# Optimization experiments

Hardware: AMD Instinct MI355X
Metric: run time of the kernel (lower is better)

The kernel has to match this reference:

```python
import jax, jax.numpy as jnp
import numpy as np

NUM_NODES = 100000
NUM_RELS = 500
DIM = 64          # input_dim == hidden_dim == output_dim
NUM_EDGES = 1_000_000
LEAKY_SLOPE = 0.01  # torch F.leaky_relu default


def _linear_params(key, fin, fout):
    # torch nn.Linear default init: U(-1/sqrt(fin), 1/sqrt(fin))
    kw, kb = jax.random.split(key)
    s = 1.0 / np.sqrt(fin)
    W = jax.random.uniform(kw, (fout, fin), minval=-s, maxval=s, dtype=jnp.float32)
    b = jax.random.uniform(kb, (fout,), minval=-s, maxval=s, dtype=jnp.float32)
    return W, b


def setup_inputs() -> dict:
    key = jax.random.key(0)
    ks = jax.random.split(key, 12)
    src_idx = jax.random.randint(ks[0], (NUM_EDGES,), 0, NUM_NODES, dtype=jnp.int32)
    dst_idx = jax.random.randint(ks[1], (NUM_EDGES,), 0, NUM_NODES, dtype=jnp.int32)
    rel_idx = jax.random.randint(ks[2], (NUM_EDGES,), 0, NUM_RELS, dtype=jnp.int32)
    ent_embed = jax.random.normal(ks[3], (NUM_NODES, DIM), dtype=jnp.float32)
    rel_embed = jax.random.normal(ks[4], (NUM_RELS, DIM), dtype=jnp.float32)
    W_ent, b_ent = _linear_params(ks[5], DIM, DIM)          # fc_ent
    W_relL, b_relL = _linear_params(ks[6], DIM, DIM)        # fc_rel
    W_rel2, b_rel2 = _linear_params(ks[7], DIM, DIM)        # fc_rel2
    W_rel3, b_rel3 = _linear_params(ks[8], 3 * DIM, DIM)    # fc_rel3
    W_a, b_a = _linear_params(ks[9], DIM, 1)                # a
    W_fc, b_fc = _linear_params(ks[10], 3 * DIM, DIM)       # fc
    return {
        "ent_embed": ent_embed, "rel_embed": rel_embed,
        "W_ent": W_ent, "b_ent": b_ent,
        "W_relL": W_relL, "b_relL": b_relL,
        "W_rel2": W_rel2, "b_rel2": b_rel2,
        "W_rel3": W_rel3, "b_rel3": b_rel3,
        "W_a": W_a, "b_a": b_a,
        "W_fc": W_fc, "b_fc": b_fc,
        "src_idx": src_idx, "dst_idx": dst_idx, "rel_idx": rel_idx,
    }


def reference(ent_embed, rel_embed, W_ent, b_ent, W_relL, b_relL,
              W_rel2, b_rel2, W_rel3, b_rel3, W_a, b_a, W_fc, b_fc,
              src_idx, dst_idx, rel_idx):
    # --- per-edge projections (first=True path: lookup from learned tables) ---
    src = ent_embed[src_idx] @ W_ent.T + b_ent            # [E, D]
    dst = ent_embed[dst_idx] @ W_ent.T + b_ent            # [E, D]
    rel = rel_embed[rel_idx] @ W_relL.T + b_relL          # [E, D]

    # --- edge message c and unnormalized attention b ---
    c = jnp.concatenate([src, dst, rel], axis=1) @ W_fc.T + b_fc   # [E, D]
    logits = jax.nn.leaky_relu((c @ W_a.T + b_a)[:, 0], LEAKY_SLOPE)  # [E]
    b = jnp.exp(logits)                                    # [E] (original uses plain exp)

    # --- scatter-softmax over edges grouped by source node ---
    b_sum = jax.ops.segment_sum(b, src_idx, num_segments=NUM_NODES)  # [N]
    alpha = b / b_sum[src_idx]                             # [E]

    # --- attention-weighted neighbor aggregation ---
    h_ent = jax.ops.segment_sum(alpha[:, None] * c, src_idx,
                                num_segments=NUM_NODES)    # [N, D]

    # --- relation pooling: mean over edges of each relation ---
    rel2 = rel @ W_rel2.T + b_rel2                         # [E, D]
    feats = jnp.concatenate([h_ent[src_idx], h_ent[dst_idx], rel2], axis=1)  # [E, 3D]
    sums = jax.ops.segment_sum(feats, rel_idx, num_segments=NUM_RELS)        # [R, 3D]
    counts = jax.ops.segment_sum(jnp.ones_like(b), rel_idx, num_segments=NUM_RELS)
    mean = sums / jnp.maximum(counts, 1.0)[:, None]        # [R, 3D]

    h_rel = mean @ W_rel3.T + b_rel3                       # [R, D]
    return (h_ent, h_rel)
```

## Files before the change

kernel.cpp:

```cpp
#include <hip/hip_runtime.h>
#include <hip/hip_fp16.h>
#include <math.h>

#define N_NODES 100000
#define N_RELS  500
#define DIM     64
#define N_EDGES 1000000
#define SLOPE   0.01f
#define RSUB    16
#define SC_EDGES 2048
#define NB_E    489
#define NBKT    196
#define BSH     9
#define NROWS   (N_RELS + NBKT)
#define BMAX    5632

__device__ __forceinline__ unsigned short f2bf(float f) {
    unsigned int u = __float_as_uint(f);
    u += 0x7FFFu + ((u >> 16) & 1u);
    return (unsigned short)(u >> 16);
}
__device__ __forceinline__ float bfl(unsigned int u) { return __uint_as_float(u << 16); }
__device__ __forceinline__ float bfh(unsigned int u) { return __uint_as_float(u & 0xFFFF0000u); }

__device__ __forceinline__ unsigned int f2e5m2(float f) {
    __half h = __float2half_rn(f);
    unsigned short hu;
    __builtin_memcpy(&hu, &h, 2);
    unsigned int u = hu;
    u += 0x7Fu + ((u >> 8) & 1u);
    return (u >> 8) & 0xFFu;
}
__device__ __forceinline__ float e5d(unsigned int b) {
    unsigned short u = (unsigned short)(b << 8);
    __half h;
    __builtin_memcpy(&h, &u, 2);
    return __half2float(h);
}
__device__ __forceinline__ void acc8(float* a, uint2 w) {
    unsigned int x = w.x, y = w.y;
    a[0] += e5d(x & 255u);         a[1] += e5d((x >> 8) & 255u);
    a[2] += e5d((x >> 16) & 255u); a[3] += e5d(x >> 24);
    a[4] += e5d(y & 255u);         a[5] += e5d((y >> 8) & 255u);
    a[6] += e5d((y >> 16) & 255u); a[7] += e5d(y >> 24);
}

__global__ void k_fold(const float* __restrict__ W_ent, const float* __restrict__ b_ent,
                       const float* __restrict__ W_relL, const float* __restrict__ b_relL,
                       const float* __restrict__ W_rel2, const float* __restrict__ b_rel2,
                       const float* __restrict__ W_fc, const float* __restrict__ b_fc,
                       float* __restrict__ Wcat, float* __restrict__ dcat,
                       float* __restrict__ MW, float* __restrict__ MQ,
                       float* __restrict__ dW, float* __restrict__ dQ) {
    int idx = blockIdx.x * 256 + threadIdx.x;
    if (idx < 8192) {
        int k = idx >> 7;
        int j2 = idx & 127;
        int jj = j2 & 63;
        int off = (j2 >> 6) * 64;
        float s = 0.f;
        for (int i = 0; i < 64; i++) s += W_fc[jj*192 + off + i] * W_ent[i*64 + k];
        Wcat[k*128 + j2] = s;
    } else if (idx < 12288) {
        int rem = idx - 8192;
        int j = rem >> 6, i = rem & 63;
        float s = 0.f;
        for (int k = 0; k < 64; k++) s += W_fc[j*192 + 128 + k] * W_relL[k*64 + i];
        MW[j*64 + i] = s;
    } else if (idx < 16384) {
        int rem = idx - 12288;
        int j = rem >> 6, i = rem & 63;
        float s = 0.f;
        for (int k = 0; k < 64; k++) s += W_rel2[j*64 + k] * W_relL[k*64 + i];
        MQ[j*64 + i] = s;
    } else if (idx < 16512) {
        int j2 = idx - 16384;
        int jj = j2 & 63;
        int off = (j2 >> 6) * 64;
        float s = 0.f;
        for (int i = 0; i < 64; i++) s += b_ent[i] * W_fc[jj*192 + off + i];
        dcat[j2] = s;
    } else if (idx < 16640) {
        int rem = idx - 16512;
        int vec = rem >> 6, j = rem & 63;
        if (vec == 0) {
            float s = b_fc[j];
            for (int k = 0; k < 64; k++) s += b_relL[k] * W_fc[j*192 + 128 + k];
            dW[j] = s;
        } else {
            float s = b_rel2[j];
            for (int k = 0; k < 64; k++) s += b_relL[k] * W_rel2[j*64 + k];
            dQ[j] = s;
        }
    }
}

__global__ __launch_bounds__(256) void k_node(const float* __restrict__ ent,
        const float* __restrict__ Wcat, const float* __restrict__ dcat,
        const float* __restrict__ W_a,
        float* __restrict__ Uout, unsigned short* __restrict__ V16,
        float* __restrict__ us, float* __restrict__ vs) {
    __shared__ float sA[64][68];
    __shared__ float sW[64][128];
    int t = threadIdx.x;
    int tile0 = blockIdx.x * 64;
    for (int i = t; i < 2048; i += 256)
        ((float4*)sW)[i] = ((const float4*)Wcat)[i];
    for (int f = t; f < 1024; f += 256) {
        int n = f >> 4, k4 = f & 15;
        float4 v4 = (tile0 + n < N_NODES)
            ? ((const float4*)(ent + (size_t)(tile0 + n) * 64))[k4]
            : make_float4(0.f, 0.f, 0.f, 0.f);
        *(float4*)&sA[n][k4 * 4] = v4;
    }
    __syncthreads();

    int ng = t >> 4;
    int jg = t & 15;
    int n0 = ng * 4;
    int j0 = jg * 8;

    float4 d0 = *(const float4*)(dcat + j0);
    float4 d1 = *(const float4*)(dcat + j0 + 4);
    float acc[4][8];
    #pragma unroll
    for (int a = 0; a < 4; a++) {
        acc[a][0] = d0.x; acc[a][1] = d0.y; acc[a][2] = d0.z; acc[a][3] = d0.w;
        acc[a][4] = d1.x; acc[a][5] = d1.y; acc[a][6] = d1.z; acc[a][7] = d1.w;
    }

    #pragma unroll 4
    for (int k = 0; k < 64; k++) {
        float4 w0 = *(const float4*)&sW[k][j0];
        float4 w1 = *(const float4*)&sW[k][j0 + 4];
        float e0 = sA[n0][k], e1 = sA[n0+1][k], e2 = sA[n0+2][k], e3 = sA[n0+3][k];
        float e[4] = {e0, e1, e2, e3};
        #pragma unroll
        for (int a = 0; a < 4; a++) {
            acc[a][0] += e[a] * w0.x; acc[a][1] += e[a] * w0.y;
            acc[a][2] += e[a] * w0.z; acc[a][3] += e[a] * w0.w;
            acc[a][4] += e[a] * w1.x; acc[a][5] += e[a] * w1.y;
            acc[a][6] += e[a] * w1.z; acc[a][7] += e[a] * w1.w;
        }
    }

    int jw = j0 & 63;
    float4 wa0 = *(const float4*)(W_a + jw);
    float4 wa1 = *(const float4*)(W_a + jw + 4);
    float part[4];
    #pragma unroll
    for (int a = 0; a < 4; a++) {
        part[a] = acc[a][0]*wa0.x + acc[a][1]*wa0.y + acc[a][2]*wa0.z + acc[a][3]*wa0.w
                + acc[a][4]*wa1.x + acc[a][5]*wa1.y + acc[a][6]*wa1.z + acc[a][7]*wa1.w;
    }
    #pragma unroll
    for (int m = 1; m <= 4; m <<= 1) {
        #pragma unroll
        for (int a = 0; a < 4; a++) part[a] += __shfl_xor(part[a], m, 64);
    }
    if ((jg & 7) == 0) {
        float* sv = (jg < 8) ? us : vs;
        #pragma unroll
        for (int a = 0; a < 4; a++)
            if (tile0 + n0 + a < N_NODES) sv[tile0 + n0 + a] = part[a];
    }

    #pragma unroll
    for (int a = 0; a < 4; a++) {
        int n = tile0 + n0 + a;
        if (n >= N_NODES) break;
        if (jg < 8) {
            float4 o0 = make_float4(acc[a][0], acc[a][1], acc[a][2], acc[a][3]);
            float4 o1 = make_float4(acc[a][4], acc[a][5], acc[a][6], acc[a][7]);
            float* base = Uout + (size_t)n * 64 + j0;
            *(float4*)(base) = o0;
            *(float4*)(base + 4) = o1;
        } else {
            uint4 pv;
            pv.x = (unsigned int)f2bf(acc[a][0]) | ((unsigned int)f2bf(acc[a][1]) << 16);
            pv.y = (unsigned int)f2bf(acc[a][2]) | ((unsigned int)f2bf(acc[a][3]) << 16);
            pv.z = (unsigned int)f2bf(acc[a][4]) | ((unsigned int)f2bf(acc[a][5]) << 16);
            pv.w = (unsigned int)f2bf(acc[a][6]) | ((unsigned int)f2bf(acc[a][7]) << 16);
            *(uint4*)(V16 + (size_t)n * 64 + (j0 - 64)) = pv;
        }
    }
}

__global__ __launch_bounds__(256, 2) void k_relproj(const float* __restrict__ relE,
        const float* __restrict__ MW, const float* __restrict__ MQ,
        const float* __restrict__ dW, const float* __restrict__ dQ,
        const float* __restrict__ W_a,
        unsigned short* __restrict__ Wr16, float* __restrict__ Qr, float* __restrict__ wsr) {
    int lane = threadIdx.x & 63;
    int wv = threadIdx.x >> 6;
    float mw[64], mq[64];
    #pragma unroll
    for (int i = 0; i < 64; i++) { mw[i] = MW[lane*64 + i]; mq[i] = MQ[lane*64 + i]; }
    float dw = dW[lane], dq = dQ[lane], wa = W_a[lane];
    int r = blockIdx.x * 4 + wv;
    if (r >= N_RELS) return;
    float e = relE[(size_t)r * 64 + lane];
    float w = dw, q = dq;
    #pragma unroll
    for (int i = 0; i < 64; i++) {
        float ei = __shfl(e, i, 64);
        w += ei * mw[i];
        q += ei * mq[i];
    }
    Wr16[(size_t)r * 64 + lane] = f2bf(w);
    Qr[(size_t)r * 64 + lane] = q;
    float tw = w * wa;
    #pragma unroll
    for (int o = 32; o; o >>= 1) tw += __shfl_xor(tw, o, 64);
    if (lane == 0) wsr[r] = tw;
}

__global__ void k_zero(int* __restrict__ a, int n) {
    int g = blockIdx.x * 256 + threadIdx.x;
    if (g < n) a[g] = 0;
}

__global__ __launch_bounds__(256) void k_hist(const int* __restrict__ src, const int* __restrict__ rel,
        int* __restrict__ cnt_rel, int* __restrict__ bucket_cnt, int* __restrict__ blkhist) {
    __shared__ int lcntR[N_RELS];
    __shared__ int lcntS[NBKT];
    int t = threadIdx.x;
    for (int r = t; r < N_RELS; r += 256) lcntR[r] = 0;
    for (int b = t; b < NBKT; b += 256) lcntS[b] = 0;
    __syncthreads();
    int base = blockIdx.x * SC_EDGES;
    if (base + SC_EDGES <= N_EDGES) {
        int e0 = base + t * 8;
        int4 sa = *(const int4*)(src + e0);
        int4 sb = *(const int4*)(src + e0 + 4);
        int4 ra = *(const int4*)(rel + e0);
        int4 rb = *(const int4*)(rel + e0 + 4);
        atomicAdd(&lcntS[sa.x >> BSH], 1); atomicAdd(&lcntS[sa.y >> BSH], 1);
        atomicAdd(&lcntS[sa.z >> BSH], 1); atomicAdd(&lcntS[sa.w >> BSH], 1);
        atomicAdd(&lcntS[sb.x >> BSH], 1); atomicAdd(&lcntS[sb.y >> BSH], 1);
        atomicAdd(&lcntS[sb.z >> BSH], 1); atomicAdd(&lcntS[sb.w >> BSH], 1);
        atomicAdd(&lcntR[ra.x], 1); atomicAdd(&lcntR[ra.y], 1);
        atomicAdd(&lcntR[ra.z], 1); atomicAdd(&lcntR[ra.w], 1);
        atomicAdd(&lcntR[rb.x], 1); atomicAdd(&lcntR[rb.y], 1);
        atomicAdd(&lcntR[rb.z], 1); atomicAdd(&lcntR[rb.w], 1);
    } else {
        for (int g = base + t; g < N_EDGES; g += 256) {
            atomicAdd(&lcntS[src[g] >> BSH], 1);
            atomicAdd(&lcntR[rel[g]], 1);
        }
    }
    __syncthreads();
    for (int r = t; r < N_RELS; r += 256) {
        int c = lcntR[r];
        blkhist[(size_t)r * NB_E + blockIdx.x] = c;
        if (c) atomicAdd(&cnt_rel[r], c);
    }
    for (int b = t; b < NBKT; b += 256) {
        int c = lcntS[b];
        blkhist[(size_t)(N_RELS + b) * NB_E + blockIdx.x] = c;
        if (c) atomicAdd(&bucket_cnt[b], c);
    }
}

__global__ void k_scan_two(const int* __restrict__ cnt_rel, const int* __restrict__ bucket_cnt,
                           int* __restrict__ starts) {
    __shared__ int tot[256];
    int t = threadIdx.x;
    const int* cnt = blockIdx.x ? bucket_cnt : cnt_rel;
    int n = blockIdx.x ? NBKT : N_RELS;
    int* out = starts + (blockIdx.x ? N_RELS : 0);
    int myv[4];
    int mySum = 0;
    for (int q = 0; q < 4; q++) {
        int g = t * 4 + q;
        int v = (g < n) ? cnt[g] : 0;
        myv[q] = v; mySum += v;
    }
    tot[t] = mySum;
    __syncthreads();
    for (int o = 1; o < 256; o <<= 1) {
        int u = (t >= o) ? tot[t - o] : 0;
        __syncthreads();
        tot[t] += u;
        __syncthreads();
    }
    int run = tot[t] - mySum;
    for (int q = 0; q < 4; q++) {
        int g = t * 4 + q;
        if (g < n) out[g] = run;
        run += myv[q];
    }
}

__global__ __launch_bounds__(256) void k_scan_relblk(const int* __restrict__ starts,
        const int* __restrict__ blkhist, int* __restrict__ blkbase) {
    int lane = threadIdx.x & 63;
    int row = (blockIdx.x * 256 + threadIdx.x) >> 6;
    if (row >= NROWS) return;
    int run = starts[row];
    for (int base = 0; base < NB_E; base += 64) {
        int b = base + lane;
        int v = (b < NB_E) ? blkhist[(size_t)row * NB_E + b] : 0;
        int x = v;
        #pragma unroll
        for (int o = 1; o < 64; o <<= 1) {
            int y = __shfl_up(x, o, 64);
            if (lane >= o) x += y;
        }
        if (b < NB_E) blkbase[(size_t)row * NB_E + b] = run + (x - v);
        run += __shfl(x, 63, 64);
    }
}

__global__ __launch_bounds__(256) void k_scatter(const int* __restrict__ src, const int* __restrict__ dst,
        const int* __restrict__ rel, const int* __restrict__ blkbase,
        int2* __restrict__ pay_rel, int* __restrict__ stg_a, int* __restrict__ stg_b) {
    __shared__ int lbaseR[N_RELS];
    __shared__ int loffR[N_RELS];
    __shared__ int lbaseS[NBKT];
    __shared__ int loffS[NBKT];
    int t = threadIdx.x;
    for (int r = t; r < N_RELS; r += 256) {
        lbaseR[r] = blkbase[(size_t)r * NB_E + blockIdx.x];
        loffR[r] = 0;
    }
    for (int b = t; b < NBKT; b += 256) {
        lbaseS[b] = blkbase[(size_t)(N_RELS + b) * NB_E + blockIdx.x];
        loffS[b] = 0;
    }
    __syncthreads();
    int base = blockIdx.x * SC_EDGES;
    if (base + SC_EDGES <= N_EDGES) {
        int e0 = base + t * 8;
        int4 sa = *(const int4*)(src + e0);
        int4 sb = *(const int4*)(src + e0 + 4);
        int4 da = *(const int4*)(dst + e0);
        int4 db = *(const int4*)(dst + e0 + 4);
        int4 ra = *(const int4*)(rel + e0);
        int4 rb = *(const int4*)(rel + e0 + 4);
        int s[8] = {sa.x, sa.y, sa.z, sa.w, sb.x, sb.y, sb.z, sb.w};
        int d[8] = {da.x, da.y, da.z, da.w, db.x, db.y, db.z, db.w};
        int r8[8] = {ra.x, ra.y, ra.z, ra.w, rb.x, rb.y, rb.z, rb.w};
        int p[8], q[8];
        #pragma unroll
        for (int j = 0; j < 8; j++) q[j] = lbaseR[r8[j]] + atomicAdd(&loffR[r8[j]], 1);
        #pragma unroll
        for (int j = 0; j < 8; j++) p[j] = lbaseS[s[j] >> BSH] + atomicAdd(&loffS[s[j] >> BSH], 1);
        #pragma unroll
        for (int j = 0; j < 8; j++) pay_rel[q[j]] = make_int2(s[j], d[j]);
        #pragma unroll
        for (int j = 0; j < 8; j++) stg_a[p[j]] = d[j];
        #pragma unroll
        for (int j = 0; j < 8; j++) stg_b[p[j]] = ((s[j] & 511) << 9) | r8[j];
    } else {
        for (int g = base + t; g < N_EDGES; g += 256) {
            int s = src[g], d = dst[g], r = rel[g];
            int q = lbaseR[r] + atomicAdd(&loffR[r], 1);
            pay_rel[q] = make_int2(s, d);
            int sb2 = s >> BSH;
            int p = lbaseS[sb2] + atomicAdd(&loffS[sb2], 1);
            stg_a[p] = d;
            stg_b[p] = ((s & 511) << 9) | r;
        }
    }
}

__global__ __launch_bounds__(256) void k_sortb(const int* __restrict__ stg_a,
        const int* __restrict__ stg_b, const int* __restrict__ starts,
        const int* __restrict__ bucket_cnt,
        const float* __restrict__ us, const float* __restrict__ vs,
        const float* __restrict__ wsr, const float* __restrict__ b_a_p,
        int2* __restrict__ pay_src, float* __restrict__ pay_b,
        int* __restrict__ start_src, int* __restrict__ cnt_src,
        float* __restrict__ bsum_arr) {
    __shared__ int hist[512];
    __shared__ int lstart[512];
    __shared__ int loff[512];
    __shared__ int tot[256];
    __shared__ float lbsum[512];
    __shared__ int2 lpay[BMAX];
    int bkt = blockIdx.x;
    int base = starts[N_RELS + bkt];
    int n = bucket_cnt[bkt];
    int t = threadIdx.x;
    float ba = b_a_p[0];
    hist[t] = 0; hist[t + 256] = 0;
    lbsum[t] = 0.f; lbsum[t + 256] = 0.f;
    __syncthreads();
    for (int i = t; i < n; i += 256)
        atomicAdd(&hist[stg_b[base + i] >> 9], 1);
    __syncthreads();
    int v0 = hist[t * 2], v1 = hist[t * 2 + 1];
    int mySum = v0 + v1;
    tot[t] = mySum;
    __syncthreads();
    for (int o = 1; o < 256; o <<= 1) {
        int u = (t >= o) ? tot[t - o] : 0;
        __syncthreads();
        tot[t] += u;
        __syncthreads();
    }
    int run = tot[t] - mySum;
    lstart[t * 2] = run;
    lstart[t * 2 + 1] = run + v0;
    loff[t * 2] = 0;
    loff[t * 2 + 1] = 0;
    int node0 = bkt * 512 + t * 2;
    if (node0 < N_NODES) { start_src[node0] = base + run; cnt_src[node0] = v0; }
    if (node0 + 1 < N_NODES) { start_src[node0 + 1] = base + run + v0; cnt_src[node0 + 1] = v1; }
    __syncthreads();
    bool fits = (n <= BMAX);
    for (int i = t; i < n; i += 256) {
        int bb = stg_b[base + i];
        int d = stg_a[base + i];
        int lo = bb >> 9;
        int pos = lstart[lo] + atomicAdd(&loff[lo], 1);
        if (fits) {
            lpay[pos] = make_int2(d, bb);
        } else {
            int r = bb & 511;
            int s = bkt * 512 + lo;
            float t0 = us[s] + vs[d] + wsr[r] + ba;
            t0 = t0 > 0.f ? t0 : SLOPE * t0;
            float b = expf(t0);
            pay_src[base + pos] = make_int2(d, r);
            pay_b[base + pos] = b;
            atomicAdd(&lbsum[lo], b);
        }
    }
    __syncthreads();
    if (fits) {
        for (int i = t; i < n; i += 256) {
            int2 pr = lpay[i];
            int bb = pr.y;
            int lo = bb >> 9;
            int r = bb & 511;
            int s = bkt * 512 + lo;
            float t0 = us[s] + vs[pr.x] + wsr[r] + ba;
            t0 = t0 > 0.f ? t0 : SLOPE * t0;
            float b = expf(t0);
            pay_src[base + i] = make_int2(pr.x, r);
            pay_b[base + i] = b;
            atomicAdd(&lbsum[lo], b);
        }
        __syncthreads();
    }
    if (node0 < N_NODES) bsum_arr[node0] = lbsum[t * 2];
    if (node0 + 1 < N_NODES) bsum_arr[node0 + 1] = lbsum[t * 2 + 1];
}

__global__ __launch_bounds__(256) void k_attn(const int2* __restrict__ pay,
        const float* __restrict__ pay_b,
        const int* __restrict__ start_src, const int* __restrict__ cnt_src,
        const float* __restrict__ bsum_arr,
        const unsigned short* __restrict__ V16, const unsigned short* __restrict__ Wr16,
        float* __restrict__ h, unsigned char* __restrict__ h8) {
    int lane = threadIdx.x & 63;
    int wv = threadIdx.x >> 6;
    int quarter = lane >> 4;
    int lq = lane & 15;
    int slot = lq >> 3;
    int li = lq & 7;
    int n = blockIdx.x * 16 + wv * 4 + quarter;
    if (n >= N_NODES) return;
    int st = start_src[n];
    int cnt = cnt_src[n];
    if (cnt == 0) {
        if (lq < 8) {
            float* hp = h + (size_t)n * 64 + lq * 8;
            *(float4*)hp = make_float4(0.f, 0.f, 0.f, 0.f);
            *(float4*)(hp + 4) = make_float4(0.f, 0.f, 0.f, 0.f);
            *(uint2*)(h8 + (size_t)n * 64 + lq * 8) = make_uint2(0u, 0u);
        }
        return;
    }
    float inv = 1.f / bsum_arr[n];
    float a[8] = {0.f, 0.f, 0.f, 0.f, 0.f, 0.f, 0.f, 0.f};
    for (int e = slot; e < cnt; e += 4) {
        int eB = e + 2;
        bool vB = eB < cnt;
        int eBc = vB ? eB : e;
        float bA = pay_b[st + e];
        float bB = vB ? pay_b[st + eB] : 0.f;
        int2 pA = pay[st + e];
        int2 pB = pay[st + eBc];
        uint4 vvA = *(const uint4*)(V16 + (size_t)pA.x * 64 + li * 8);
        uint4 wwA = *(const uint4*)(Wr16 + (size_t)pA.y * 64 + li * 8);
        uint4 vvB = *(const uint4*)(V16 + (size_t)pB.x * 64 + li * 8);
        uint4 wwB = *(const uint4*)(Wr16 + (size_t)pB.y * 64 + li * 8);
        a[0] += bA * (bfl(vvA.x) + bfl(wwA.x)) + bB * (bfl(vvB.x) + bfl(wwB.x));
        a[1] += bA * (bfh(vvA.x) + bfh(wwA.x)) + bB * (bfh(vvB.x) + bfh(wwB.x));
        a[2] += bA * (bfl(vvA.y) + bfl(wwA.y)) + bB * (bfl(vvB.y) + bfl(wwB.y));
        a[3] += bA * (bfh(vvA.y) + bfh(wwA.y)) + bB * (bfh(vvB.y) + bfh(wwB.y));
        a[4] += bA * (bfl(vvA.z) + bfl(wwA.z)) + bB * (bfl(vvB.z) + bfl(wwB.z));
        a[5] += bA * (bfh(vvA.z) + bfh(wwA.z)) + bB * (bfh(vvB.z) + bfh(wwB.z));
        a[6] += bA * (bfl(vvA.w) + bfl(wwA.w)) + bB * (bfl(vvB.w) + bfl(wwB.w));
        a[7] += bA * (bfh(vvA.w) + bfh(wwA.w)) + bB * (bfh(vvB.w) + bfh(wwB.w));
    }
    #pragma unroll
    for (int d = 0; d < 8; d++) a[d] += __shfl_xor(a[d], 8, 64);
    if (slot == 0) {
        float* hp = h + (size_t)n * 64 + li * 8;
        float o[8];
        #pragma unroll
        for (int d = 0; d < 8; d++) o[d] = hp[d] + a[d] * inv;
        *(float4*)hp = make_float4(o[0], o[1], o[2], o[3]);
        *(float4*)(hp + 4) = make_float4(o[4], o[5], o[6], o[7]);
        uint2 p8;
        p8.x = f2e5m2(o[0]) | (f2e5m2(o[1]) << 8) | (f2e5m2(o[2]) << 16) | (f2e5m2(o[3]) << 24);
        p8.y = f2e5m2(o[4]) | (f2e5m2(o[5]) << 8) | (f2e5m2(o[6]) << 16) | (f2e5m2(o[7]) << 24);
        *(uint2*)(h8 + (size_t)n * 64 + li * 8) = p8;
    }
}

__global__ __launch_bounds__(256) void k_relpool(const int2* __restrict__ pay,
        const int* __restrict__ start_rel, const int* __restrict__ cnt_rel,
        const unsigned char* __restrict__ h8, float* __restrict__ acc_rel) {
    int r = blockIdx.x / RSUB;
    int sub = blockIdx.x % RSUB;
    int st = start_rel[r];
    int cnt = cnt_rel[r];
    int t = threadIdx.x;
    int j = t >> 4;
    int side = (t >> 3) & 1;
    int li = t & 7;

    int chunk = (cnt + RSUB - 1) / RSUB;
    int k0 = sub * chunk;
    int k1 = min(k0 + chunk, cnt);
    int len = k1 - k0;

    float a[8] = {0.f,0.f,0.f,0.f,0.f,0.f,0.f,0.f};
    if (len > 0) {
        const int2* pp = pay + st + k0;
        for (int base = 0; base < len; base += 64) {
            int m[4]; bool v[4]; int2 p[4];
            #pragma unroll
            for (int s = 0; s < 4; s++) {
                m[s] = base + j + s * 16;
                v[s] = m[s] < len;
                p[s] = v[s] ? pp[m[s]] : make_int2(0, 0);
            }
            uint2 hv[4];
            #pragma unroll
            for (int s = 0; s < 4; s++) {
                int idx = side ? p[s].y : p[s].x;
                hv[s] = *(const uint2*)(h8 + (size_t)idx * 64 + li * 8);
            }
            #pragma unroll
            for (int s = 0; s < 4; s++) if (v[s]) acc8(a, hv[s]);
        }
    }
    __shared__ float red[256][9];
    #pragma unroll
    for (int d = 0; d < 8; d++) red[t][d] = a[d];
    __syncthreads();
    #pragma unroll
    for (int off = 128; off >= 16; off >>= 1) {
        if (t < off) {
            #pragma unroll
            for (int d = 0; d < 8; d++) red[t][d] += red[t + off][d];
        }
        __syncthreads();
    }
    if (t < 16) {
        int sd = (t >> 3) & 1;
        int ll = t & 7;
        float* dstp = &acc_rel[r * 128 + sd * 64 + ll * 8];
        #pragma unroll
        for (int d = 0; d < 8; d++) atomicAdd(dstp + d, red[t][d]);
    }
}

__global__ void k_relfin(const float* __restrict__ acc_rel, const int* __restrict__ cnt_rel,
                         const float* __restrict__ Qr, const float* __restrict__ W_rel3,
                         const float* __restrict__ b_rel3, float* __restrict__ out) {
    int g = blockIdx.x * 256 + threadIdx.x;
    if (g >= N_RELS * 64) return;
    int r = g >> 6;
    int j = g & 63;
    int cnt = cnt_rel[r];
    float invc = 1.f / (float)(cnt > 0 ? cnt : 1);
    float s = b_rel3[j];
    for (int k = 0; k < 128; k++) s += acc_rel[r * 128 + k] * invc * W_rel3[j * 192 + k];
    if (cnt > 0)
        for (int k = 0; k < 64; k++) s += Qr[r * 64 + k] * W_rel3[j * 192 + 128 + k];
    out[g] = s;
}

extern "C" void kernel_launch(void* const* d_in, const int* in_sizes, int n_in,
                              void* d_out, int out_size, void* d_ws, size_t ws_size,
                              hipStream_t stream) {
    const float* ent    = (const float*)d_in[0];
    const float* relE   = (const float*)d_in[1];
    const float* W_ent  = (const float*)d_in[2];
    const float* b_ent  = (const float*)d_in[3];
    const float* W_relL = (const float*)d_in[4];
    const float* b_relL = (const float*)d_in[5];
    const float* W_rel2 = (const float*)d_in[6];
    const float* b_rel2 = (const float*)d_in[7];
    const float* W_rel3 = (const float*)d_in[8];
    const float* b_rel3 = (const float*)d_in[9];
    const float* W_a    = (const float*)d_in[10];
    const float* b_a    = (const float*)d_in[11];
    const float* W_fc   = (const float*)d_in[12];
    const float* b_fc   = (const float*)d_in[13];
    const int* src = (const int*)d_in[14];
    const int* dst = (const int*)d_in[15];
    const int* rel = (const int*)d_in[16];
    float* out = (float*)d_out;

    char* ws = (char*)d_ws;
    size_t off = 0;
    auto alloc = [&](size_t bytes) -> void* {
        void* p = ws + off;
        off += (bytes + 255) & ~(size_t)255;
        return p;
    };
    float* Wcat = (float*)alloc(8192 * 4);
    float* dcat = (float*)alloc(128 * 4);
    float* MW  = (float*)alloc(4096 * 4);
    float* MQ  = (float*)alloc(4096 * 4);
    float* dW  = (float*)alloc(64 * 4);
    float* dQ  = (float*)alloc(64 * 4);
    unsigned short* V16 = (unsigned short*)alloc((size_t)N_NODES * 64 * 2);
    unsigned char* h8 = (unsigned char*)alloc((size_t)N_NODES * 64);
    float* us  = (float*)alloc((size_t)N_NODES * 4);
    float* vs  = (float*)alloc((size_t)N_NODES * 4);
    unsigned short* Wr16 = (unsigned short*)alloc((size_t)N_RELS * 64 * 2);
    float* Qr  = (float*)alloc((size_t)N_RELS * 64 * 4);
    float* wsr = (float*)alloc((size_t)N_RELS * 4);
    int* cnt_src   = (int*)alloc((size_t)N_NODES * 4);
    int* start_src = (int*)alloc((size_t)N_NODES * 4);
    float* bsum    = (float*)alloc((size_t)N_NODES * 4);
    int* cnts      = (int*)alloc((size_t)NROWS * 4);
    int* starts    = (int*)alloc((size_t)NROWS * 4);
    int* blkhist   = (int*)alloc((size_t)NROWS * NB_E * 4);
    int* blkbase   = (int*)alloc((size_t)NROWS * NB_E * 4);
    int* stg_a     = (int*)alloc((size_t)N_EDGES * 4);
    int* stg_b     = (int*)alloc((size_t)N_EDGES * 4);
    int2* pay_src  = (int2*)alloc((size_t)N_EDGES * 8);
    float* pay_b   = (float*)alloc((size_t)N_EDGES * 4);
    int2* pay_rel  = (int2*)alloc((size_t)N_EDGES * 8);
    float* acc_rel = (float*)alloc((size_t)N_RELS * 128 * 4);

    int* cnt_rel    = cnts;
    int* bucket_cnt = cnts + N_RELS;

    k_zero<<<(NROWS + 255) / 256, 256, 0, stream>>>(cnts, NROWS);
    k_zero<<<(N_RELS * 128 + 255) / 256, 256, 0, stream>>>((int*)acc_rel, N_RELS * 128);

    k_fold<<<65, 256, 0, stream>>>(W_ent, b_ent, W_relL, b_relL, W_rel2, b_rel2,
                                   W_fc, b_fc, Wcat, dcat, MW, MQ, dW, dQ);
    k_node<<<(N_NODES + 63) / 64, 256, 0, stream>>>(ent, Wcat, dcat, W_a, out, V16, us, vs);
    k_relproj<<<125, 256, 0, stream>>>(relE, MW, MQ, dW, dQ, W_a, Wr16, Qr, wsr);
    k_hist<<<NB_E, 256, 0, stream>>>(src, rel, cnt_rel, bucket_cnt, blkhist);
    k_scan_two<<<2, 256, 0, stream>>>(cnt_rel, bucket_cnt, starts);
    k_scan_relblk<<<(NROWS * 64 + 255) / 256, 256, 0, stream>>>(starts, blkhist, blkbase);
    k_scatter<<<NB_E, 256, 0, stream>>>(src, dst, rel, blkbase, pay_rel, stg_a, stg_b);
    k_sortb<<<NBKT, 256, 0, stream>>>(stg_a, stg_b, starts, bucket_cnt,
                                      us, vs, wsr, b_a,
                                      pay_src, pay_b, start_src, cnt_src, bsum);
    k_attn<<<(N_NODES + 15) / 16, 256, 0, stream>>>(pay_src, pay_b, start_src, cnt_src,
                                                    bsum, V16, Wr16, out, h8);
    k_relpool<<<N_RELS * RSUB, 256, 0, stream>>>(pay_rel, starts, cnt_rel, h8, acc_rel);
    k_relfin<<<(N_RELS * 64 + 255) / 256, 256, 0, stream>>>(acc_rel, cnt_rel, Qr, W_rel3,
                                                            b_rel3, out + (size_t)N_NODES * 64);
}
```

Measured before the change: 316.9 us.

## Widen relpool gathers to 16 bytes, prefetch payload, use shuffle reduction

Rewrites the relation-pooling kernel so each thread gathers 16-byte chunks of the fp8 node rows instead of 8 bytes, and each block handles 128 edges per iteration. The next iteration's payload indices are software-prefetched while the current gathers are in flight. The shared-memory tree reduction with many syncthreads is replaced by wave shuffles plus one small cross-wave sum, and RSUB drops from 16 to 4 so there are fewer blocks and fewer atomics per relation. In exchange there is less parallelism per relation and higher register use.

```diff
diff --git a/kernel.cpp b/kernel.cpp
--- a/kernel.cpp
+++ b/kernel.cpp
@@ -7,7 +7,7 @@
 #define DIM     64
 #define N_EDGES 1000000
 #define SLOPE   0.01f
-#define RSUB    16
+#define RSUB    4
 #define SC_EDGES 2048
 #define NB_E    489
 #define NBKT    196
@@ -37,12 +37,15 @@
     __builtin_memcpy(&h, &u, 2);
     return __half2float(h);
 }
-__device__ __forceinline__ void acc8(float* a, uint2 w) {
-    unsigned int x = w.x, y = w.y;
+__device__ __forceinline__ void acc8(float* a, unsigned int x, unsigned int y) {
     a[0] += e5d(x & 255u);         a[1] += e5d((x >> 8) & 255u);
     a[2] += e5d((x >> 16) & 255u); a[3] += e5d(x >> 24);
     a[4] += e5d(y & 255u);         a[5] += e5d((y >> 8) & 255u);
     a[6] += e5d((y >> 16) & 255u); a[7] += e5d(y >> 24);
+}
+__device__ __forceinline__ void acc16(float* a, uint4 w) {
+    acc8(a, w.x, w.y);
+    acc8(a + 8, w.z, w.w);
 }
 
 __global__ void k_fold(const float* __restrict__ W_ent, const float* __restrict__ b_ent,
@@ -521,54 +524,71 @@
     int st = start_rel[r];
     int cnt = cnt_rel[r];
     int t = threadIdx.x;
-    int j = t >> 4;
-    int side = (t >> 3) & 1;
-    int li = t & 7;
+    int li = t & 3;
+    int side = (t >> 2) & 1;
+    int j = t >> 3;
 
     int chunk = (cnt + RSUB - 1) / RSUB;
     int k0 = sub * chunk;
     int k1 = min(k0 + chunk, cnt);
     int len = k1 - k0;
 
-    float a[8] = {0.f,0.f,0.f,0.f,0.f,0.f,0.f,0.f};
+    float a[16];
+    #pragma unroll
+    for (int d = 0; d < 16; d++) a[d] = 0.f;
+
     if (len > 0) {
         const int2* pp = pay + st + k0;
-        for (int base = 0; base < len; base += 64) {
-            int m[4]; bool v[4]; int2 p[4];
-            #pragma unroll
-            for (int s = 0; s < 4; s++) {
-                m[s] = base + j + s * 16;
-                v[s] = m[s] < len;
-                p[s] = v[s] ? pp[m[s]] : make_int2(0, 0);
-            }
-            uint2 hv[4];
+        int m[4]; bool v[4]; int2 p[4];
+        #pragma unroll
+        for (int s = 0; s < 4; s++) {
+            m[s] = j + s * 32;
+            v[s] = m[s] < len;
+            p[s] = v[s] ? pp[m[s]] : make_int2(0, 0);
+        }
+        for (int base = 0; base < len; base += 128) {
+            uint4 hv[4];
             #pragma unroll
             for (int s = 0; s < 4; s++) {
                 int idx = side ? p[s].y : p[s].x;
-                hv[s] = *(const uint2*)(h8 + (size_t)idx * 64 + li * 8);
+                hv[s] = *(const uint4*)(h8 + (size_t)idx * 64 + li * 16);
+            }
+            int mn[4]; bool vn[4]; int2 pn[4];
+            #pragma unroll
+            for (int s = 0; s < 4; s++) {
+                mn[s] = m[s] + 128;
+                vn[s] = mn[s] < len;
+                pn[s] = vn[s] ? pp[mn[s]] : make_int2(0, 0);
             }
             #pragma unroll
-            for (int s = 0; s < 4; s++) if (v[s]) acc8(a, hv[s]);
-        }
-    }
-    __shared__ float red[256][9];
-    #pragma unroll
-    for (int d = 0; d < 8; d++) red[t][d] = a[d];
-    __syncthreads();
-    #pragma unroll
-    for (int off = 128; off >= 16; off >>= 1) {
-        if (t < off) {
+            for (int s = 0; s < 4; s++) if (v[s]) acc16(a, hv[s]);
             #pragma unroll
-            for (int d = 0; d < 8; d++) red[t][d] += red[t + off][d];
-        }
-        __syncthreads();
-    }
-    if (t < 16) {
-        int sd = (t >> 3) & 1;
-        int ll = t & 7;
-        float* dstp = &acc_rel[r * 128 + sd * 64 + ll * 8];
-        #pragma unroll
-        for (int d = 0; d < 8; d++) atomicAdd(dstp + d, red[t][d]);
+            for (int s = 0; s < 4; s++) { m[s] = mn[s]; v[s] = vn[s]; p[s] = pn[s]; }
+        }
+    }
+
+    #pragma unroll
+    for (int d = 0; d < 16; d++) {
+        a[d] += __shfl_xor(a[d], 8, 64);
+        a[d] += __shfl_xor(a[d], 16, 64);
+        a[d] += __shfl_xor(a[d], 32, 64);
+    }
+
+    __shared__ float red[4][8][16];
+    int wv = t >> 6;
+    int lane = t & 63;
+    if (lane < 8) {
+        #pragma unroll
+        for (int d = 0; d < 16; d++) red[wv][lane][d] = a[d];
+    }
+    __syncthreads();
+    if (t < 128) {
+        int sl = t >> 4;
+        int d = t & 15;
+        float s = red[0][sl][d] + red[1][sl][d] + red[2][sl][d] + red[3][sl][d];
+        int sd = sl >> 2;
+        int li2 = sl & 3;
+        atomicAdd(&acc_rel[r * 128 + sd * 64 + li2 * 16 + d], s);
     }
 }
 
```

After: 302.5 us. -4.5%, faster.

## Replace relation-sorted pooling with node-bucketed LDS accumulation and partial reduction

Applied to the files above, without the earlier changes.

The relation pooling no longer sorts edges by relation with a per-relation gather. Edges are now bucketed by both src and dst node ranges, so the h8 gathers in the pool kernel read nodes in near-sequential order. Each block accumulates into a 500x64 float table in LDS with shared atomics, writes bf16 partials, and a separate kernel reduces them. This removes the relation-key histogram and scatter and the random h8 reads, but adds a dst-bucket scatter pass, heavy LDS atomic contention, a 125KB LDS footprint per block, and bf16 rounding of the partial sums.

```diff
diff --git a/kernel.cpp b/kernel.cpp
--- a/kernel.cpp
+++ b/kernel.cpp
@@ -7,13 +7,14 @@
 #define DIM     64
 #define N_EDGES 1000000
 #define SLOPE   0.01f
-#define RSUB    16
 #define SC_EDGES 2048
 #define NB_E    489
 #define NBKT    196
 #define BSH     9
-#define NROWS   (N_RELS + NBKT)
+#define NRB     (2 * NBKT)
 #define BMAX    5632
+#define POOL_BLKS 128
+#define POOL_SLOTS 32000
 
 __device__ __forceinline__ unsigned short f2bf(float f) {
     unsigned int u = __float_as_uint(f);
@@ -36,13 +37,6 @@
     __half h;
     __builtin_memcpy(&h, &u, 2);
     return __half2float(h);
-}
-__device__ __forceinline__ void acc8(float* a, uint2 w) {
-    unsigned int x = w.x, y = w.y;
-    a[0] += e5d(x & 255u);         a[1] += e5d((x >> 8) & 255u);
-    a[2] += e5d((x >> 16) & 255u); a[3] += e5d(x >> 24);
-    a[4] += e5d(y & 255u);         a[5] += e5d((y >> 8) & 255u);
-    a[6] += e5d((y >> 16) & 255u); a[7] += e5d(y >> 24);
 }
 
 __global__ void k_fold(const float* __restrict__ W_ent, const float* __restrict__ b_ent,
@@ -220,25 +214,34 @@
     if (g < n) a[g] = 0;
 }
 
-__global__ __launch_bounds__(256) void k_hist(const int* __restrict__ src, const int* __restrict__ rel,
-        int* __restrict__ cnt_rel, int* __restrict__ bucket_cnt, int* __restrict__ blkhist) {
+__global__ __launch_bounds__(256) void k_hist(const int* __restrict__ src,
+        const int* __restrict__ dst, const int* __restrict__ rel,
+        int* __restrict__ cnt_rel, int* __restrict__ bktS, int* __restrict__ bktD,
+        int* __restrict__ blkhist) {
     __shared__ int lcntR[N_RELS];
     __shared__ int lcntS[NBKT];
+    __shared__ int lcntD[NBKT];
     int t = threadIdx.x;
     for (int r = t; r < N_RELS; r += 256) lcntR[r] = 0;
-    for (int b = t; b < NBKT; b += 256) lcntS[b] = 0;
+    for (int b = t; b < NBKT; b += 256) { lcntS[b] = 0; lcntD[b] = 0; }
     __syncthreads();
     int base = blockIdx.x * SC_EDGES;
     if (base + SC_EDGES <= N_EDGES) {
         int e0 = base + t * 8;
         int4 sa = *(const int4*)(src + e0);
         int4 sb = *(const int4*)(src + e0 + 4);
+        int4 da = *(const int4*)(dst + e0);
+        int4 db = *(const int4*)(dst + e0 + 4);
         int4 ra = *(const int4*)(rel + e0);
         int4 rb = *(const int4*)(rel + e0 + 4);
         atomicAdd(&lcntS[sa.x >> BSH], 1); atomicAdd(&lcntS[sa.y >> BSH], 1);
         atomicAdd(&lcntS[sa.z >> BSH], 1); atomicAdd(&lcntS[sa.w >> BSH], 1);
         atomicAdd(&lcntS[sb.x >> BSH], 1); atomicAdd(&lcntS[sb.y >> BSH], 1);
         atomicAdd(&lcntS[sb.z >> BSH], 1); atomicAdd(&lcntS[sb.w >> BSH], 1);
+        atomicAdd(&lcntD[da.x >> BSH], 1); atomicAdd(&lcntD[da.y >> BSH], 1);
+        atomicAdd(&lcntD[da.z >> BSH], 1); atomicAdd(&lcntD[da.w >> BSH], 1);
+        atomicAdd(&lcntD[db.x >> BSH], 1); atomicAdd(&lcntD[db.y >> BSH], 1);
+        atomicAdd(&lcntD[db.z >> BSH], 1); atomicAdd(&lcntD[db.w >> BSH], 1);
         atomicAdd(&lcntR[ra.x], 1); atomicAdd(&lcntR[ra.y], 1);
         atomicAdd(&lcntR[ra.z], 1); atomicAdd(&lcntR[ra.w], 1);
         atomicAdd(&lcntR[rb.x], 1); atomicAdd(&lcntR[rb.y], 1);
@@ -246,29 +249,32 @@
     } else {
         for (int g = base + t; g < N_EDGES; g += 256) {
             atomicAdd(&lcntS[src[g] >> BSH], 1);
+            atomicAdd(&lcntD[dst[g] >> BSH], 1);
             atomicAdd(&lcntR[rel[g]], 1);
         }
     }
     __syncthreads();
     for (int r = t; r < N_RELS; r += 256) {
         int c = lcntR[r];
-        blkhist[(size_t)r * NB_E + blockIdx.x] = c;
         if (c) atomicAdd(&cnt_rel[r], c);
     }
     for (int b = t; b < NBKT; b += 256) {
-        int c = lcntS[b];
-        blkhist[(size_t)(N_RELS + b) * NB_E + blockIdx.x] = c;
-        if (c) atomicAdd(&bucket_cnt[b], c);
-    }
-}
-
-__global__ void k_scan_two(const int* __restrict__ cnt_rel, const int* __restrict__ bucket_cnt,
+        int cs = lcntS[b];
+        blkhist[(size_t)b * NB_E + blockIdx.x] = cs;
+        if (cs) atomicAdd(&bktS[b], cs);
+        int cd = lcntD[b];
+        blkhist[(size_t)(NBKT + b) * NB_E + blockIdx.x] = cd;
+        if (cd) atomicAdd(&bktD[b], cd);
+    }
+}
+
+__global__ void k_scan_two(const int* __restrict__ bktS, const int* __restrict__ bktD,
                            int* __restrict__ starts) {
     __shared__ int tot[256];
     int t = threadIdx.x;
-    const int* cnt = blockIdx.x ? bucket_cnt : cnt_rel;
-    int n = blockIdx.x ? NBKT : N_RELS;
-    int* out = starts + (blockIdx.x ? N_RELS : 0);
+    const int* cnt = blockIdx.x ? bktD : bktS;
+    int n = NBKT;
+    int* out = starts + (blockIdx.x ? NBKT : 0);
     int myv[4];
     int mySum = 0;
     for (int q = 0; q < 4; q++) {
@@ -296,7 +302,7 @@
         const int* __restrict__ blkhist, int* __restrict__ blkbase) {
     int lane = threadIdx.x & 63;
     int row = (blockIdx.x * 256 + threadIdx.x) >> 6;
-    if (row >= NROWS) return;
+    if (row >= NRB) return;
     int run = starts[row];
     for (int base = 0; base < NB_E; base += 64) {
         int b = base + lane;
@@ -314,19 +320,17 @@
 
 __global__ __launch_bounds__(256) void k_scatter(const int* __restrict__ src, const int* __restrict__ dst,
         const int* __restrict__ rel, const int* __restrict__ blkbase,
-        int2* __restrict__ pay_rel, int* __restrict__ stg_a, int* __restrict__ stg_b) {
-    __shared__ int lbaseR[N_RELS];
-    __shared__ int loffR[N_RELS];
+        int* __restrict__ stg_a, int* __restrict__ stg_b, int* __restrict__ stg_c) {
     __shared__ int lbaseS[NBKT];
     __shared__ int loffS[NBKT];
+    __shared__ int lbaseD[NBKT];
+    __shared__ int loffD[NBKT];
     int t = threadIdx.x;
-    for (int r = t; r < N_RELS; r += 256) {
-        lbaseR[r] = blkbase[(size_t)r * NB_E + blockIdx.x];
-        loffR[r] = 0;
-    }
     for (int b = t; b < NBKT; b += 256) {
-        lbaseS[b] = blkbase[(size_t)(N_RELS + b) * NB_E + blockIdx.x];
+        lbaseS[b] = blkbase[(size_t)b * NB_E + blockIdx.x];
         loffS[b] = 0;
+        lbaseD[b] = blkbase[(size_t)(NBKT + b) * NB_E + blockIdx.x];
+        loffD[b] = 0;
     }
     __syncthreads();
     int base = blockIdx.x * SC_EDGES;
@@ -343,24 +347,25 @@
         int r8[8] = {ra.x, ra.y, ra.z, ra.w, rb.x, rb.y, rb.z, rb.w};
         int p[8], q[8];
         #pragma unroll
-        for (int j = 0; j < 8; j++) q[j] = lbaseR[r8[j]] + atomicAdd(&loffR[r8[j]], 1);
-        #pragma unroll
         for (int j = 0; j < 8; j++) p[j] = lbaseS[s[j] >> BSH] + atomicAdd(&loffS[s[j] >> BSH], 1);
         #pragma unroll
-        for (int j = 0; j < 8; j++) pay_rel[q[j]] = make_int2(s[j], d[j]);
+        for (int j = 0; j < 8; j++) q[j] = lbaseD[d[j] >> BSH] + atomicAdd(&loffD[d[j] >> BSH], 1);
         #pragma unroll
         for (int j = 0; j < 8; j++) stg_a[p[j]] = d[j];
         #pragma unroll
-        for (int j = 0; j < 8; j++) stg_b[p[j]] = ((s[j] & 511) << 9) | r8[j];
+        for (int j = 0; j < 8; j++) stg_b[p[j]] = (s[j] << 9) | r8[j];
+        #pragma unroll
+        for (int j = 0; j < 8; j++) stg_c[q[j]] = (d[j] << 9) | r8[j];
     } else {
         for (int g = base + t; g < N_EDGES; g += 256) {
             int s = src[g], d = dst[g], r = rel[g];
-            int q = lbaseR[r] + atomicAdd(&loffR[r], 1);
-            pay_rel[q] = make_int2(s, d);
             int sb2 = s >> BSH;
             int p = lbaseS[sb2] + atomicAdd(&loffS[sb2], 1);
             stg_a[p] = d;
-            stg_b[p] = ((s & 511) << 9) | r;
+            stg_b[p] = (s << 9) | r;
+            int db2 = d >> BSH;
+            int q = lbaseD[db2] + atomicAdd(&loffD[db2], 1);
+            stg_c[q] = (d << 9) | r;
         }
     }
 }
@@ -380,7 +385,7 @@
     __shared__ float lbsum[512];
     __shared__ int2 lpay[BMAX];
     int bkt = blockIdx.x;
-    int base = starts[N_RELS + bkt];
+    int base = starts[bkt];
     int n = bucket_cnt[bkt];
     int t = threadIdx.x;
     float ba = b_a_p[0];
@@ -388,7 +393,7 @@
     lbsum[t] = 0.f; lbsum[t + 256] = 0.f;
     __syncthreads();
     for (int i = t; i < n; i += 256)
-        atomicAdd(&hist[stg_b[base + i] >> 9], 1);
+        atomicAdd(&hist[(stg_b[base + i] >> 9) & 511], 1);
     __syncthreads();
     int v0 = hist[t * 2], v1 = hist[t * 2 + 1];
     int mySum = v0 + v1;
@@ -413,7 +418,7 @@
     for (int i = t; i < n; i += 256) {
         int bb = stg_b[base + i];
         int d = stg_a[base + i];
-        int lo = bb >> 9;
+        int lo = (bb >> 9) & 511;
         int pos = lstart[lo] + atomicAdd(&loff[lo], 1);
         if (fits) {
             lpay[pos] = make_int2(d, bb);
@@ -433,7 +438,7 @@
         for (int i = t; i < n; i += 256) {
             int2 pr = lpay[i];
             int bb = pr.y;
-            int lo = bb >> 9;
+            int lo = (bb >> 9) & 511;
             int r = bb & 511;
             int s = bkt * 512 + lo;
             float t0 = us[s] + vs[pr.x] + wsr[r] + ba;
@@ -513,63 +518,73 @@
     }
 }
 
-__global__ __launch_bounds__(256) void k_relpool(const int2* __restrict__ pay,
-        const int* __restrict__ start_rel, const int* __restrict__ cnt_rel,
-        const unsigned char* __restrict__ h8, float* __restrict__ acc_rel) {
-    int r = blockIdx.x / RSUB;
-    int sub = blockIdx.x % RSUB;
-    int st = start_rel[r];
-    int cnt = cnt_rel[r];
+__global__ __launch_bounds__(1024) void k_pool(const int* __restrict__ stg_b,
+        const int* __restrict__ stg_c, const unsigned char* __restrict__ h8,
+        unsigned int* __restrict__ part) {
+    __shared__ float acc[POOL_SLOTS];
     int t = threadIdx.x;
-    int j = t >> 4;
-    int side = (t >> 3) & 1;
-    int li = t & 7;
-
-    int chunk = (cnt + RSUB - 1) / RSUB;
-    int k0 = sub * chunk;
-    int k1 = min(k0 + chunk, cnt);
-    int len = k1 - k0;
-
-    float a[8] = {0.f,0.f,0.f,0.f,0.f,0.f,0.f,0.f};
-    if (len > 0) {
-        const int2* pp = pay + st + k0;
-        for (int base = 0; base < len; base += 64) {
-            int m[4]; bool v[4]; int2 p[4];
-            #pragma unroll
-            for (int s = 0; s < 4; s++) {
-                m[s] = base + j + s * 16;
-                v[s] = m[s] < len;
-                p[s] = v[s] ? pp[m[s]] : make_int2(0, 0);
-            }
-            uint2 hv[4];
-            #pragma unroll
-            for (int s = 0; s < 4; s++) {
-                int idx = side ? p[s].y : p[s].x;
-                hv[s] = *(const uint2*)(h8 + (size_t)idx * 64 + li * 8);
-            }
-            #pragma unroll
-            for (int s = 0; s < 4; s++) if (v[s]) acc8(a, hv[s]);
-        }
-    }
-    __shared__ float red[256][9];
-    #pragma unroll
-    for (int d = 0; d < 8; d++) red[t][d] = a[d];
-    __syncthreads();
-    #pragma unroll
-    for (int off = 128; off >= 16; off >>= 1) {
-        if (t < off) {
-            #pragma unroll
-            for (int d = 0; d < 8; d++) red[t][d] += red[t + off][d];
-        }
-        __syncthreads();
-    }
-    if (t < 16) {
-        int sd = (t >> 3) & 1;
-        int ll = t & 7;
-        float* dstp = &acc_rel[r * 128 + sd * 64 + ll * 8];
-        #pragma unroll
-        for (int d = 0; d < 8; d++) atomicAdd(dstp + d, red[t][d]);
-    }
+    for (int i = t; i < POOL_SLOTS; i += 1024) acc[i] = 0.f;
+    __syncthreads();
+    int side = blockIdx.x >> 7;
+    int idx  = blockIdx.x & 127;
+    const int* stream = side ? stg_c : stg_b;
+    const int chunk = (N_EDGES + POOL_BLKS - 1) / POOL_BLKS;
+    int lo = idx * chunk;
+    int hi = lo + chunk; if (hi > N_EDGES) hi = N_EDGES;
+    int lane = t & 63;
+    int wv = t >> 6;
+    for (int pos = lo + wv * 64; pos < hi; pos += 16 * 64) {
+        int lim = hi - pos; if (lim > 64) lim = 64;
+        int ebatch = (lane < lim) ? stream[pos + lane] : 0;
+        int j = 0;
+        for (; j + 4 <= lim; j += 4) {
+            int e0 = __builtin_amdgcn_readlane(ebatch, j);
+            int e1 = __builtin_amdgcn_readlane(ebatch, j + 1);
+            int e2 = __builtin_amdgcn_readlane(ebatch, j + 2);
+            int e3 = __builtin_amdgcn_readlane(ebatch, j + 3);
+            unsigned int b0 = h8[(size_t)(e0 >> 9) * 64 + lane];
+            unsigned int b1 = h8[(size_t)(e1 >> 9) * 64 + lane];
+            unsigned int b2 = h8[(size_t)(e2 >> 9) * 64 + lane];
+            unsigned int b3 = h8[(size_t)(e3 >> 9) * 64 + lane];
+            atomicAdd(&acc[(e0 & 511) * 64 + lane], e5d(b0));
+            atomicAdd(&acc[(e1 & 511) * 64 + lane], e5d(b1));
+            atomicAdd(&acc[(e2 & 511) * 64 + lane], e5d(b2));
+            atomicAdd(&acc[(e3 & 511) * 64 + lane], e5d(b3));
+        }
+        for (; j < lim; j++) {
+            int e0 = __builtin_amdgcn_readlane(ebatch, j);
+            unsigned int b0 = h8[(size_t)(e0 >> 9) * 64 + lane];
+            atomicAdd(&acc[(e0 & 511) * 64 + lane], e5d(b0));
+        }
+    }
+    __syncthreads();
+    unsigned int* pb = part + (size_t)blockIdx.x * (POOL_SLOTS / 2);
+    for (int i = t; i < POOL_SLOTS / 2; i += 1024) {
+        unsigned int u = (unsigned int)f2bf(acc[2 * i])
+                       | ((unsigned int)f2bf(acc[2 * i + 1]) << 16);
+        pb[i] = u;
+    }
+}
+
+__global__ __launch_bounds__(256) void k_polred(const unsigned int* __restrict__ part,
+        float* __restrict__ acc_rel) {
+    int g = blockIdx.x * 256 + threadIdx.x;
+    if (g >= POOL_SLOTS) return;
+    int side = g / (POOL_SLOTS / 2);
+    int slot = g % (POOL_SLOTS / 2);
+    const unsigned int* p = part + (size_t)side * POOL_BLKS * (POOL_SLOTS / 2) + slot;
+    float s0 = 0.f, s1 = 0.f;
+    #pragma unroll 8
+    for (int k = 0; k < POOL_BLKS; k++) {
+        unsigned int u = p[(size_t)k * (POOL_SLOTS / 2)];
+        s0 += bfl(u);
+        s1 += bfh(u);
+    }
+    int f0 = 2 * slot;
+    int r = f0 >> 6;
+    int d = f0 & 63;
+    acc_rel[r * 128 + side * 64 + d] = s0;
+    acc_rel[r * 128 + side * 64 + d + 1] = s1;
 }
 
 __global__ void k_relfin(const float* __restrict__ acc_rel, const int* __restrict__ cnt_rel,
@@ -633,37 +648,39 @@
     int* cnt_src   = (int*)alloc((size_t)N_NODES * 4);
     int* start_src = (int*)alloc((size_t)N_NODES * 4);
     float* bsum    = (float*)alloc((size_t)N_NODES * 4);
-    int* cnts      = (int*)alloc((size_t)NROWS * 4);
-    int* starts    = (int*)alloc((size_t)NROWS * 4);
-    int* blkhist   = (int*)alloc((size_t)NROWS * NB_E * 4);
-    int* blkbase   = (int*)alloc((size_t)NROWS * NB_E * 4);
+    int* cnts      = (int*)alloc((size_t)(N_RELS + NRB) * 4);
+    int* starts    = (int*)alloc((size_t)NRB * 4);
+    int* blkhist   = (int*)alloc((size_t)NRB * NB_E * 4);
+    int* blkbase   = (int*)alloc((size_t)NRB * NB_E * 4);
     int* stg_a     = (int*)alloc((size_t)N_EDGES * 4);
     int* stg_b     = (int*)alloc((size_t)N_EDGES * 4);
+    int* stg_c     = (int*)alloc((size_t)N_EDGES * 4);
     int2* pay_src  = (int2*)alloc((size_t)N_EDGES * 8);
     float* pay_b   = (float*)alloc((size_t)N_EDGES * 4);
-    int2* pay_rel  = (int2*)alloc((size_t)N_EDGES * 8);
+    unsigned int* part = (unsigned int*)alloc((size_t)2 * POOL_BLKS * (POOL_SLOTS / 2) * 4);
     float* acc_rel = (float*)alloc((size_t)N_RELS * 128 * 4);
 
-    int* cnt_rel    = cnts;
-    int* bucket_cnt = cnts + N_RELS;
-
-    k_zero<<<(NROWS + 255) / 256, 256, 0, stream>>>(cnts, NROWS);
-    k_zero<<<(N_RELS * 128 + 255) / 256, 256, 0, stream>>>((int*)acc_rel, N_RELS * 128);
+    int* cnt_rel = cnts;
+    int* bktS    = cnts + N_RELS;
+    int* bktD    = cnts + N_RELS + NBKT;
+
+    k_zero<<<(N_RELS + NRB + 255) / 256, 256, 0, stream>>>(cnts, N_RELS + NRB);
 
     k_fold<<<65, 256, 0, stream>>>(W_ent, b_ent, W_relL, b_relL, W_rel2, b_rel2,
                                    W_fc, b_fc, Wcat, dcat, MW, MQ, dW, dQ);
     k_node<<<(N_NODES + 63) / 64, 256, 0, stream>>>(ent, Wcat, dcat, W_a, out, V16, us, vs);
     k_relproj<<<125, 256, 0, stream>>>(relE, MW, MQ, dW, dQ, W_a, Wr16, Qr, wsr);
-    k_hist<<<NB_E, 256, 0, stream>>>(src, rel, cnt_rel, bucket_cnt, blkhist);
-    k_scan_two<<<2, 256, 0, stream>>>(cnt_rel, bucket_cnt, starts);
-    k_scan_relblk<<<(NROWS * 64 + 255) / 256, 256, 0, stream>>>(starts, blkhist, blkbase);
-    k_scatter<<<NB_E, 256, 0, stream>>>(src, dst, rel, blkbase, pay_rel, stg_a, stg_b);
-    k_sortb<<<NBKT, 256, 0, stream>>>(stg_a, stg_b, starts, bucket_cnt,
+    k_hist<<<NB_E, 256, 0, stream>>>(src, dst, rel, cnt_rel, bktS, bktD, blkhist);
+    k_scan_two<<<2, 256, 0, stream>>>(bktS, bktD, starts);
+    k_scan_relblk<<<(NRB * 64 + 255) / 256, 256, 0, stream>>>(starts, blkhist, blkbase);
+    k_scatter<<<NB_E, 256, 0, stream>>>(src, dst, rel, blkbase, stg_a, stg_b, stg_c);
+    k_sortb<<<NBKT, 256, 0, stream>>>(stg_a, stg_b, starts, bktS,
                                       us, vs, wsr, b_a,
                                       pay_src, pay_b, start_src, cnt_src, bsum);
     k_attn<<<(N_NODES + 15) / 16, 256, 0, stream>>>(pay_src, pay_b, start_src, cnt_src,
                                                     bsum, V16, Wr16, out, h8);
-    k_relpool<<<N_RELS * RSUB, 256, 0, stream>>>(pay_rel, starts, cnt_rel, h8, acc_rel);
+    k_pool<<<2 * POOL_BLKS, 1024, 0, stream>>>(stg_b, stg_c, h8, part);
+    k_polred<<<(POOL_SLOTS + 255) / 256, 256, 0, stream>>>(part, acc_rel);
     k_relfin<<<(N_RELS * 64 + 255) / 256, 256, 0, stream>>>(acc_rel, cnt_rel, Qr, W_rel3,
                                                             b_rel3, out + (size_t)N_NODES * 64);
 }
```

Result: slower. 900.1 us (+184.1%).
